# Kernel tuning notes

Hardware: AMD Instinct MI355X
Metric: run time of the kernel (lower is better)

The kernel has to match this reference:

```python
import jax, jax.numpy as jnp
import numpy as np

B = 8192        # number of drug-cell pairs (graphs)
NPG = 32        # nodes per graph
EPG = 64        # directed edges per graph
N = B * NPG     # total nodes
E = B * EPG     # total edges
CELL = 908      # cell_inp_dim
BN_EPS = 1e-5


def _bn(x):
    # BatchNorm1d in training mode with gamma=1, beta=0 (fresh init), biased var
    m = x.mean(0)
    v = x.var(0)
    return (x - m) * jax.lax.rsqrt(v + BN_EPS)


def _lin_params(k, fan_in, fan_out):
    kw, _ = jax.random.split(k)
    w = jax.random.normal(kw, (fan_in, fan_out), jnp.float32) / np.sqrt(fan_in)
    b = jnp.zeros((fan_out,), jnp.float32)
    return w, b


_DIMS = [("ce_1", CELL, 516), ("ce_2", 516, 256), ("ce_3", 256, 128),
         ("g1_1", 9, 128), ("g1_2", 128, 128),
         ("g2_1", 128, 128), ("g2_2", 128, 128),
         ("d_1", 128, 128), ("d_2", 128, 128),
         ("f_1", 256, 128), ("f_2", 128, 64), ("f_3", 64, 1)]


def setup_inputs() -> dict:
    key = jax.random.key(0)
    ks = jax.random.split(key, 4 + len(_DIMS))
    inp = {}
    inp["cell"] = jax.random.normal(ks[0], (B, CELL), jnp.float32)
    inp["drug_x"] = jax.random.normal(ks[1], (N, 9), jnp.float32)
    g = jnp.arange(E) // EPG  # graph id per edge
    src = g * NPG + jax.random.randint(ks[2], (E,), 0, NPG)
    dst = g * NPG + jax.random.randint(ks[3], (E,), 0, NPG)
    inp["drug_edge_index"] = jnp.stack([src, dst]).astype(jnp.int32)
    inp["drug_batch"] = (jnp.arange(N) // NPG).astype(jnp.int32)
    for i, (nm, a, b) in enumerate(_DIMS):
        w, bb = _lin_params(ks[4 + i], a, b)
        inp[nm + "_w"] = w
        inp[nm + "_b"] = bb
    return inp


def _forward(cell, drug_x, src, dst, batch,
             ce_1_w, ce_1_b, ce_2_w, ce_2_b, ce_3_w, ce_3_b,
             g1_1_w, g1_1_b, g1_2_w, g1_2_b,
             g2_1_w, g2_1_b, g2_2_w, g2_2_b,
             d_1_w, d_1_b, d_2_w, d_2_b,
             f_1_w, f_1_b, f_2_w, f_2_b, f_3_w, f_3_b):
    # cell_emb branch (dropout = identity in eval/reference)
    c = jax.nn.relu(_bn(cell @ ce_1_w + ce_1_b))
    c = jax.nn.relu(_bn(c @ ce_2_w + ce_2_b))
    c = jax.nn.relu(_bn(c @ ce_3_w + ce_3_b))

    # GINConv 1: h = MLP((1+eps)*x + sum_{j in N(i)} x_j), eps=0
    agg = jax.ops.segment_sum(drug_x[src], dst, num_segments=N)
    h = drug_x + agg
    h = jax.nn.relu(_bn(h @ g1_1_w + g1_1_b)) @ g1_2_w + g1_2_b  # inner MLP: Lin-BN-ReLU-Lin
    h = _bn(jax.nn.relu(h))  # outer ReLU then BN (per Sequential order)

    # GINConv 2
    agg = jax.ops.segment_sum(h[src], dst, num_segments=N)
    h = h + agg
    h = jax.nn.relu(_bn(h @ g2_1_w + g2_1_b)) @ g2_2_w + g2_2_b
    h = _bn(jax.nn.relu(h))

    # global max pool over nodes of each graph -> [B, 128]
    p = jax.ops.segment_max(h, batch, num_segments=B)

    d = jax.nn.relu(_bn(p @ d_1_w + d_1_b))
    d = jax.nn.relu(d @ d_2_w + d_2_b)

    z = jnp.concatenate([c, d], axis=-1)  # [B, 256]
    z = jax.nn.elu(_bn(z @ f_1_w + f_1_b))
    z = jax.nn.elu(_bn(z @ f_2_w + f_2_b))
    y = (z @ f_3_w + f_3_b).reshape(B)
    return y


def reference(cell, drug_x, drug_edge_index, drug_batch,
              ce_1_w, ce_1_b, ce_2_w, ce_2_b, ce_3_w, ce_3_b,
              g1_1_w, g1_1_b, g1_2_w, g1_2_b,
              g2_1_w, g2_1_b, g2_2_w, g2_2_b,
              d_1_w, d_1_b, d_2_w, d_2_b,
              f_1_w, f_1_b, f_2_w, f_2_b, f_3_w, f_3_b):
    src, dst = drug_edge_index[0], drug_edge_index[1]
    return _forward(cell, drug_x, src, dst, drug_batch,
                    ce_1_w, ce_1_b, ce_2_w, ce_2_b, ce_3_w, ce_3_b,
                    g1_1_w, g1_1_b, g1_2_w, g1_2_b,
                    g2_1_w, g2_1_b, g2_2_w, g2_2_b,
                    d_1_w, d_1_b, d_2_w, d_2_b,
                    f_1_w, f_1_b, f_2_w, f_2_b, f_3_w, f_3_b)
```

## Files before the change

kernel.cpp:

```cpp
#include <hip/hip_runtime.h>
#include <hip/hip_bf16.h>
#include <math.h>

#define BGRAPH 8192
#define NPG 32
#define EPG 64
#define NNODE (BGRAPH * NPG)
#define NEDGE (BGRAPH * EPG)
#define CELLD 908
#define BN_EPS 1e-5f
#define ABF_STR 1024
#define C1_STR 640

typedef __attribute__((ext_vector_type(8))) short bf16x8;
typedef __attribute__((ext_vector_type(4))) float f32x4;
typedef __attribute__((ext_vector_type(4))) unsigned short us4;
typedef __attribute__((ext_vector_type(8))) unsigned short us8;

__device__ __forceinline__ unsigned short f2bf(float f)
{
    unsigned int u = __float_as_uint(f);
    u = (u + 0x7FFFu + ((u >> 16) & 1u)) >> 16;
    return (unsigned short)u;
}

__device__ __forceinline__ bf16x8 quant8(const float v[8])
{
    union { bf16x8 b; unsigned short u[8]; } fr;
    #pragma unroll
    for (int j = 0; j < 8; ++j) fr.u[j] = f2bf(v[j]);
    return fr.b;
}

__device__ __forceinline__ void bf2f8(bf16x8 b, float v[8])
{
    union { bf16x8 bb; unsigned short u[8]; } x; x.bb = b;
    #pragma unroll
    for (int j = 0; j < 8; ++j) v[j] = __uint_as_float((unsigned)x.u[j] << 16);
}

__device__ __forceinline__ float apply_in(float v, int mode, float mn, float iv)
{
    if (mode == 1)      { v = (v - mn) * iv; v = fmaxf(v, 0.f); }
    else if (mode == 2) { v = (v - mn) * iv; v = (v > 0.f) ? v : expm1f(v); }
    else if (mode == 3) { v = fmaxf(v, 0.f); v = (v - mn) * iv; }
    return v;
}

struct TransArgs {
    const float* w[11];
    unsigned short* wt[11];
    int K[11], N[11], ntN[11];
    int off[12];
};

__global__ void transpose_w(TransArgs a)
{
    __shared__ float t[64][65];
    int b = blockIdx.x, tid = threadIdx.x;
    int s = 0;
    while (s < 10 && b >= a.off[s + 1]) ++s;
    int t0 = b - a.off[s];
    int K = a.K[s], N = a.N[s], ntn = a.ntN[s];
    int kt = t0 / ntn, nt = t0 - kt * ntn;
    int k0 = kt * 64, n0 = nt * 64;
    const float* w = a.w[s];
    unsigned short* wt = a.wt[s];
    int c = tid & 63, rg = tid >> 6;
    #pragma unroll
    for (int i = 0; i < 16; ++i) {
        int rr = rg * 16 + i;
        int k = k0 + rr, n = n0 + c;
        t[c][rr] = (k < K && n < N) ? w[(size_t)k * N + n] : 0.f;
    }
    __syncthreads();
    #pragma unroll
    for (int i = 0; i < 16; ++i) {
        int rr = rg * 16 + i;
        int n = n0 + rr, k = k0 + c;
        if (n < N && k < K) wt[(size_t)n * K + k] = f2bf(t[rr][c]);
    }
}

struct SetupArgs {
    float* zb; int zTotal; int zBlocks;
    const int* src; const int* dst; int* row_start; int* col_idx;
};

__global__ void setup_all(SetupArgs a)
{
    int b = blockIdx.x;
    int tid = threadIdx.x;
    if (b < a.zBlocks) {
        int i = b * 256 + tid;
        if (i < a.zTotal) a.zb[i] = 0.f;
        return;
    }
    b -= a.zBlocks;
    __shared__ int cnt[4][32], fill[4][32], rsl[4][33];
    int gl = tid >> 6, e = tid & 63;
    int g = b * 4 + gl;
    if (e < 32) { cnt[gl][e] = 0; fill[gl][e] = 0; }
    __syncthreads();
    int s = a.src[g * EPG + e] - g * NPG;
    int d = a.dst[g * EPG + e] - g * NPG;
    atomicAdd(&cnt[gl][d], 1);
    __syncthreads();
    if (e == 0) {
        int acc = 0;
        for (int i = 0; i < 32; ++i) { rsl[gl][i] = acc; acc += cnt[gl][i]; }
        rsl[gl][32] = acc;
    }
    __syncthreads();
    int pos = rsl[gl][d] + atomicAdd(&fill[gl][d], 1);
    a.col_idx[g * EPG + pos] = s;
    if (e < 33) a.row_start[g * 33 + e] = rsl[gl][e];
}

__global__ void quant_cell(const float* __restrict__ cell, unsigned short* __restrict__ abf)
{
    int i = blockIdx.x * 256 + threadIdx.x;
    int row = i / (ABF_STR / 4), c4 = i - row * (ABF_STR / 4);
    int k = c4 * 4;
    us4 w = (us4){0, 0, 0, 0};
    if (k < CELLD) {
        float4 f = *(const float4*)&cell[(size_t)row * CELLD + k];
        w = (us4){ f2bf(f.x), f2bf(f.y), f2bf(f.z), f2bf(f.w) };
    }
    *(us4*)&abf[(size_t)row * ABF_STR + k] = w;
}

__global__ void quant_c1(const float* __restrict__ c1, const float* __restrict__ stats,
                         float inv_sM, unsigned short* __restrict__ out)
{
    int i = blockIdx.x * 256 + threadIdx.x;
    int row = i / (C1_STR / 4), c4 = i - row * (C1_STR / 4);
    int k = c4 * 4;
    us4 w = (us4){0, 0, 0, 0};
    if (k < 516) {
        float4 f = *(const float4*)&c1[(size_t)row * 516 + k];
        float v[4] = {f.x, f.y, f.z, f.w};
        #pragma unroll
        for (int j = 0; j < 4; ++j) {
            float s = stats[k + j], ss = stats[516 + k + j];
            float mn = s * inv_sM;
            float iv = rsqrtf(ss * inv_sM - mn * mn + BN_EPS);
            v[j] = fmaxf((v[j] - mn) * iv, 0.f);
        }
        w = (us4){ f2bf(v[0]), f2bf(v[1]), f2bf(v[2]), f2bf(v[3]) };
    }
    *(us4*)&out[(size_t)row * C1_STR + k] = w;
}

__global__ void reduce_stats(const float* __restrict__ part, int nrows, int nt,
                             float* __restrict__ out)
{
    int c = threadIdx.x;
    int per = nrows >> 6;
    int r0 = blockIdx.x * per;
    bool isq = (c >= 128);
    int cc = isq ? c - 128 : c;
    if (cc >= nt) return;
    float s = 0.f;
    for (int r = 0; r < per; ++r) s += part[(size_t)(r0 + r) * 256 + c];
    unsafeAtomicAdd(&out[(isq ? nt : 0) + cc], s);
}

#define HBS 136

__launch_bounds__(256)
__global__ void gin_s1(const float* __restrict__ drug_x,
                       const int* __restrict__ row_start,
                       const int* __restrict__ col_idx,
                       const unsigned short* __restrict__ W11,
                       const float* __restrict__ b11,
                       unsigned short* uout,
                       float* __restrict__ part)
{
    __shared__ __align__(16) unsigned short h[4 * 32 * HBS];
    __shared__ __align__(16) unsigned char ubuf[4096];
    __shared__ int rs[4][36];
    __shared__ int ci[4][64];

    unsigned short* w11l = (unsigned short*)ubuf;
    float* red = (float*)ubuf;

    int tid  = threadIdx.x;
    int wave = tid >> 6;
    int lane = tid & 63;
    int quad = lane >> 4;
    int l16  = lane & 15;
    int g0   = blockIdx.x * 4;
    unsigned short* hw = h + wave * (32 * HBS);
    float* xw = (float*)hw;

    for (int i = tid; i < 128 * 16; i += 256) {
        int n = i >> 4, k = i & 15;
        w11l[i] = (k < 9) ? W11[n * 9 + k] : (unsigned short)0;
    }
    if (tid < 132) {
        int gl = tid / 33, idx = tid - gl * 33;
        rs[gl][idx] = row_start[(g0 + gl) * 33 + idx];
    }
    {
        int gl = tid >> 6, e = tid & 63;
        ci[gl][e] = col_idx[(g0 + gl) * EPG + e];
    }
    {
        const float* xg = drug_x + (size_t)(g0 + wave) * 32 * 9;
        for (int i = lane; i < 32 * 16; i += 64) {
            int rr = i >> 4, c = i & 15;
            xw[i] = (c < 9) ? xg[rr * 9 + c] : 0.f;
        }
    }
    __syncthreads();

    f32x4 acc[2][8];
    #pragma unroll
    for (int i = 0; i < 2; ++i)
        #pragma unroll
        for (int j = 0; j < 8; ++j)
            acc[i][j] = (f32x4){0.f, 0.f, 0.f, 0.f};

    {
        bf16x8 af[2];
        #pragma unroll
        for (int mt = 0; mt < 2; ++mt) {
            int rowl = mt * 16 + l16;
            float v[8] = {0, 0, 0, 0, 0, 0, 0, 0};
            if (quad < 2) {
                float4 lo = *(const float4*)&xw[rowl * 16 + quad * 8];
                float4 hi = *(const float4*)&xw[rowl * 16 + quad * 8 + 4];
                v[0] = lo.x; v[1] = lo.y; v[2] = lo.z; v[3] = lo.w;
                v[4] = hi.x; v[5] = hi.y; v[6] = hi.z; v[7] = hi.w;
                int e0 = rs[wave][rowl], e1 = rs[wave][rowl + 1];
                for (int e = e0; e < e1; ++e) {
                    int sr = ci[wave][e];
                    float4 l2 = *(const float4*)&xw[sr * 16 + quad * 8];
                    float4 h2 = *(const float4*)&xw[sr * 16 + quad * 8 + 4];
                    v[0] += l2.x; v[1] += l2.y; v[2] += l2.z; v[3] += l2.w;
                    v[4] += h2.x; v[5] += h2.y; v[6] += h2.z; v[7] += h2.w;
                }
            }
            af[mt] = quant8(v);
        }
        #pragma unroll
        for (int nt = 0; nt < 8; ++nt) {
            bf16x8 b;
            if (quad < 2) b = *(const bf16x8*)(const void*)&w11l[(nt * 16 + l16) * 16 + quad * 8];
            else { float z[8] = {0,0,0,0,0,0,0,0}; b = quant8(z); }
            acc[0][nt] = __builtin_amdgcn_mfma_f32_16x16x32_bf16(af[0], b, acc[0][nt], 0, 0, 0);
            acc[1][nt] = __builtin_amdgcn_mfma_f32_16x16x32_bf16(af[1], b, acc[1][nt], 0, 0, 0);
        }
    }

    float ls[8], lq[8];
    unsigned short* ub = uout + (size_t)(g0 + wave) * 32 * 128;
    #pragma unroll
    for (int nt = 0; nt < 8; ++nt) {
        int col = nt * 16 + l16;
        float bv = b11[col];
        float s0 = 0.f, q0 = 0.f;
        #pragma unroll
        for (int mt = 0; mt < 2; ++mt) {
            int rb = mt * 16 + quad * 4;
            #pragma unroll
            for (int r = 0; r < 4; ++r) {
                float u = acc[mt][nt][r] + bv;
                ub[(size_t)(rb + r) * 128 + col] = f2bf(u);
                s0 += u; q0 += u * u;
            }
        }
        ls[nt] = s0; lq[nt] = q0;
    }
    __syncthreads();
    #pragma unroll
    for (int nt = 0; nt < 8; ++nt) {
        float s = ls[nt], q = lq[nt];
        s += __shfl_xor(s, 16); q += __shfl_xor(q, 16);
        s += __shfl_xor(s, 32); q += __shfl_xor(q, 32);
        if (quad == 0) {
            int col = nt * 16 + l16;
            red[(wave * 2 + 0) * 128 + col] = s;
            red[(wave * 2 + 1) * 128 + col] = q;
        }
    }
    __syncthreads();
    if (tid < 128) {
        float s = red[0 * 128 + tid] + red[2 * 128 + tid] + red[4 * 128 + tid] + red[6 * 128 + tid];
        float q = red[1 * 128 + tid] + red[3 * 128 + tid] + red[5 * 128 + tid] + red[7 * 128 + tid];
        part[(size_t)blockIdx.x * 256 + tid] = s;
        part[(size_t)blockIdx.x * 256 + 128 + tid] = q;
    }
}

__launch_bounds__(256)
__global__ void gin_s3f(const unsigned short* __restrict__ uin,
                        const int* __restrict__ row_start,
                        const int* __restrict__ col_idx,
                        const unsigned short* __restrict__ Wt,
                        const float* __restrict__ bias,
                        const float* __restrict__ in_stats, float inv_sM,
                        unsigned short* __restrict__ uout,
                        float* __restrict__ part)
{
    __shared__ __align__(16) unsigned short wsl[128 * 136];
    __shared__ float pmv[256];
    __shared__ int rs[2][33];
    __shared__ int ci[2][64];
    float* zt = (float*)wsl;

    int tid  = threadIdx.x;
    int wave = tid >> 6;
    int lane = tid & 63;
    int quad = lane >> 4;
    int l16  = lane & 15;
    int g0   = blockIdx.x * 2;
    int row0 = blockIdx.x * 64;

    if (tid < 128) {
        float s = in_stats[tid], ss = in_stats[128 + tid];
        float mn = s * inv_sM;
        pmv[tid] = mn;
        pmv[128 + tid] = rsqrtf(ss * inv_sM - mn * mn + BN_EPS);
    }
    if (tid < 66) {
        int gl = tid / 33, idx = tid - gl * 33;
        rs[gl][idx] = row_start[(g0 + gl) * 33 + idx];
    }
    if (tid >= 128) {
        int t = tid - 128;
        ci[t >> 6][t & 63] = col_idx[(g0 + (t >> 6)) * EPG + (t & 63)];
    }
    for (int i = tid; i < 128 * 32; i += 256) {
        int n = i >> 5, k = (i & 31) * 4;
        *(us4*)&wsl[n * 136 + k] = *(const us4*)&Wt[(size_t)n * 128 + k];
    }
    __syncthreads();

    bf16x8 afrag[4];
    {
        const unsigned short* ap = uin + (size_t)(row0 + wave * 16 + l16) * 128;
        #pragma unroll
        for (int ks = 0; ks < 4; ++ks) {
            int kb = ks * 32 + quad * 8;
            float v[8];
            bf2f8(*(const bf16x8*)(const void*)&ap[kb], v);
            #pragma unroll
            for (int j = 0; j < 8; ++j)
                v[j] = (fmaxf(v[j], 0.f) - pmv[kb + j]) * pmv[128 + kb + j];
            afrag[ks] = quant8(v);
        }
    }

    f32x4 acc[8];
    #pragma unroll
    for (int j = 0; j < 8; ++j) acc[j] = (f32x4){0.f, 0.f, 0.f, 0.f};
    #pragma unroll
    for (int ks = 0; ks < 4; ++ks) {
        int kb = ks * 32 + quad * 8;
        #pragma unroll
        for (int nt = 0; nt < 8; ++nt) {
            bf16x8 b = *(const bf16x8*)(const void*)&wsl[(nt * 16 + l16) * 136 + kb];
            acc[nt] = __builtin_amdgcn_mfma_f32_16x16x32_bf16(afrag[ks], b, acc[nt], 0, 0, 0);
        }
    }
    __syncthreads();

    #pragma unroll
    for (int nt = 0; nt < 8; ++nt) {
        int col = nt * 16 + l16;
        #pragma unroll
        for (int r = 0; r < 4; ++r)
            zt[(wave * 16 + quad * 4 + r) * 132 + col] = acc[nt][r];
    }
    __syncthreads();

    float sv[4] = {0.f, 0.f, 0.f, 0.f}, qv[4] = {0.f, 0.f, 0.f, 0.f};
    {
        int c4  = (tid & 31) * 4;
        int rg  = tid >> 5;
        int hh  = rg >> 2;
        int rb0 = (rg & 3) * 8;
        float4 bv = *(const float4*)&bias[c4];
        unsigned short* ub = uout + (size_t)row0 * 128;
        for (int rr = 0; rr < 8; ++rr) {
            int r = rb0 + rr;
            int lr = hh * 32 + r;
            float4 val = *(const float4*)&zt[lr * 132 + c4];
            int e0 = rs[hh][r], e1 = rs[hh][r + 1];
            for (int e = e0; e < e1; ++e) {
                float4 zz = *(const float4*)&zt[(hh * 32 + ci[hh][e]) * 132 + c4];
                val.x += zz.x; val.y += zz.y; val.z += zz.z; val.w += zz.w;
            }
            float u0 = val.x + bv.x, u1 = val.y + bv.y;
            float u2 = val.z + bv.z, u3 = val.w + bv.w;
            *(us4*)&ub[(size_t)lr * 128 + c4] =
                (us4){ f2bf(u0), f2bf(u1), f2bf(u2), f2bf(u3) };
            sv[0] += u0; sv[1] += u1; sv[2] += u2; sv[3] += u3;
            qv[0] += u0 * u0; qv[1] += u1 * u1; qv[2] += u2 * u2; qv[3] += u3 * u3;
        }
    }
    __syncthreads();
    {
        int c4 = (tid & 31) * 4, rg = tid >> 5;
        #pragma unroll
        for (int j = 0; j < 4; ++j) {
            zt[rg * 128 + c4 + j] = sv[j];
            zt[1024 + rg * 128 + c4 + j] = qv[j];
        }
    }
    __syncthreads();
    if (tid < 128) {
        float s = 0.f, q = 0.f;
        #pragma unroll
        for (int rg = 0; rg < 8; ++rg) {
            s += zt[rg * 128 + tid];
            q += zt[1024 + rg * 128 + tid];
        }
        part[(size_t)blockIdx.x * 256 + tid] = s;
        part[(size_t)blockIdx.x * 256 + 128 + tid] = q;
    }
}

template<int DO_POOL>
__launch_bounds__(256)
__global__ void gin_lin(const unsigned short* __restrict__ uin,
                        const unsigned short* __restrict__ Wt,
                        const float* __restrict__ bias,
                        const float* __restrict__ in_stats, float inv_sM,
                        unsigned short* uout,
                        float* __restrict__ part,
                        float* __restrict__ pool_out)
{
    __shared__ __align__(16) unsigned short Ws_l[128 * 136];
    __shared__ float pmv[256];
    __shared__ float red[4][2][128];

    int tid  = threadIdx.x;
    int wave = tid >> 6;
    int lane = tid & 63;
    int quad = lane >> 4;
    int l16  = lane & 15;
    int row0 = blockIdx.x * 64;

    for (int i = tid; i < 128 * 32; i += 256) {
        int n = i >> 5, k = (i & 31) * 4;
        *(us4*)&Ws_l[n * 136 + k] = *(const us4*)&Wt[(size_t)n * 128 + k];
    }
    if (tid < 128) {
        float s = in_stats[tid], ss = in_stats[128 + tid];
        float mn = s * inv_sM;
        pmv[tid] = mn;
        pmv[128 + tid] = rsqrtf(ss * inv_sM - mn * mn + BN_EPS);
    }
    __syncthreads();

    bf16x8 afrag[4];
    {
        const unsigned short* ap = uin + (size_t)(row0 + wave * 16 + l16) * 128;
        #pragma unroll
        for (int ks = 0; ks < 4; ++ks) {
            int kb = ks * 32 + quad * 8;
            float v[8];
            bf2f8(*(const bf16x8*)(const void*)&ap[kb], v);
            #pragma unroll
            for (int j = 0; j < 8; ++j)
                v[j] = fmaxf((v[j] - pmv[kb + j]) * pmv[128 + kb + j], 0.f);
            afrag[ks] = quant8(v);
        }
    }

    f32x4 acc[8];
    #pragma unroll
    for (int j = 0; j < 8; ++j) acc[j] = (f32x4){0.f, 0.f, 0.f, 0.f};
    #pragma unroll
    for (int ks = 0; ks < 4; ++ks) {
        int kb = ks * 32 + quad * 8;
        #pragma unroll
        for (int nt = 0; nt < 8; ++nt) {
            bf16x8 b = *(const bf16x8*)(const void*)&Ws_l[(nt * 16 + l16) * 136 + kb];
            acc[nt] = __builtin_amdgcn_mfma_f32_16x16x32_bf16(afrag[ks], b, acc[nt], 0, 0, 0);
        }
    }

    float ls[8], lq[8], lm[8];
    #pragma unroll
    for (int nt = 0; nt < 8; ++nt) {
        int col = nt * 16 + l16;
        float bv = bias[col];
        int rb = row0 + wave * 16 + quad * 4;
        float s0 = 0.f, q0 = 0.f, mx = -INFINITY;
        #pragma unroll
        for (int r = 0; r < 4; ++r) {
            float u = acc[nt][r] + bv;
            float ru = fmaxf(u, 0.f);
            s0 += ru; q0 += ru * ru;
            if (DO_POOL) mx = fmaxf(mx, ru);
            else uout[(size_t)(rb + r) * 128 + col] = f2bf(u);
        }
        ls[nt] = s0; lq[nt] = q0; lm[nt] = mx;
    }

    #pragma unroll
    for (int nt = 0; nt < 8; ++nt) {
        float s = ls[nt], q = lq[nt];
        s += __shfl_xor(s, 16); q += __shfl_xor(q, 16);
        s += __shfl_xor(s, 32); q += __shfl_xor(q, 32);
        if (quad == 0) {
            red[wave][0][nt * 16 + l16] = s;
            red[wave][1][nt * 16 + l16] = q;
        }
    }
    __syncthreads();
    if (tid < 128) {
        float s = red[0][0][tid] + red[1][0][tid] + red[2][0][tid] + red[3][0][tid];
        float q = red[0][1][tid] + red[1][1][tid] + red[2][1][tid] + red[3][1][tid];
        part[(size_t)blockIdx.x * 256 + tid] = s;
        part[(size_t)blockIdx.x * 256 + 128 + tid] = q;
    }
    if (DO_POOL) {
        __syncthreads();
        #pragma unroll
        for (int nt = 0; nt < 8; ++nt) {
            float m = lm[nt];
            m = fmaxf(m, __shfl_xor(m, 16));
            m = fmaxf(m, __shfl_xor(m, 32));
            if (quad == 0) red[wave][0][nt * 16 + l16] = m;
        }
        __syncthreads();
        {
            int gi = tid >> 7, col = tid & 127;
            float m = fmaxf(red[gi * 2][0][col], red[gi * 2 + 1][0][col]);
            pool_out[(size_t)((row0 >> 5) + gi) * 128 + col] = m;
        }
    }
}

template<int KSTEPS, int NT>
__launch_bounds__(256)
__global__ void gemm_rB(const float* __restrict__ A, const float* __restrict__ A2,
                        int lda, int K, int stats_K, int ksplit,
                        const unsigned short* __restrict__ Wt,
                        const float* __restrict__ bias, float* __restrict__ C,
                        const float* __restrict__ in_stats, float inv_sM, int in_mode,
                        float* __restrict__ part, int stats_mode, int out_act)
{
    constexpr int NSUBW = NT / 64;
    __shared__ float pm[KSTEPS * 32], pv[KSTEPS * 32];

    int tid  = threadIdx.x;
    int wave = tid >> 6;
    int lane = tid & 63;
    int quad = lane >> 4;
    int l16  = lane & 15;
    int m0   = blockIdx.x * 16;

    if (in_mode) {
        for (int k = tid; k < KSTEPS * 32; k += 256) {
            float mn = 0.f, iv = 1.f;
            if (k < stats_K) {
                float s = in_stats[k], ss = in_stats[stats_K + k];
                mn = s * inv_sM;
                float vr = ss * inv_sM - mn * mn;
                iv = rsqrtf(vr + BN_EPS);
            }
            pm[k] = mn; pv[k] = iv;
        }
        __syncthreads();
    }

    bf16x8 afrag[KSTEPS];
    {
        int row = m0 + l16;
        const float* ap = A + (size_t)row * lda;
        #pragma unroll
        for (int ks = 0; ks < KSTEPS; ++ks) {
            int kb = ks * 32 + quad * 8;
            float v[8];
            #pragma unroll
            for (int hh = 0; hh < 2; ++hh) {
                int k = kb + hh * 4;
                const float* p = (k >= ksplit) ? &A2[(size_t)row * 128 + (k - 128)]
                                               : &ap[k];
                float4 f = *(const float4*)p;
                v[hh * 4 + 0] = f.x; v[hh * 4 + 1] = f.y;
                v[hh * 4 + 2] = f.z; v[hh * 4 + 3] = f.w;
            }
            if (in_mode) {
                #pragma unroll
                for (int j = 0; j < 8; ++j)
                    v[j] = apply_in(v[j], in_mode, pm[kb + j], pv[kb + j]);
            }
            afrag[ks] = quant8(v);
        }
    }

    f32x4 acc[NSUBW];
    #pragma unroll
    for (int j = 0; j < NSUBW; ++j) acc[j] = (f32x4){0.f, 0.f, 0.f, 0.f};

    #pragma unroll
    for (int ks = 0; ks < KSTEPS; ++ks) {
        #pragma unroll
        for (int nt = 0; nt < NSUBW; ++nt) {
            int wrow = (wave * NSUBW + nt) * 16 + l16;
            bf16x8 b = *(const bf16x8*)(const void*)&Wt[(size_t)wrow * K + ks * 32 + quad * 8];
            acc[nt] = __builtin_amdgcn_mfma_f32_16x16x32_bf16(afrag[ks], b, acc[nt], 0, 0, 0);
        }
    }

    float ls[NSUBW], lq[NSUBW];
    #pragma unroll
    for (int nt = 0; nt < NSUBW; ++nt) { ls[nt] = 0.f; lq[nt] = 0.f; }

    #pragma unroll
    for (int nt = 0; nt < NSUBW; ++nt) {
        int col = (wave * NSUBW + nt) * 16 + l16;
        float bv = bias[col];
        int rbase = m0 + quad * 4;
        #pragma unroll
        for (int r = 0; r < 4; ++r) {
            float u = acc[nt][r] + bv;
            if (C) {
                float wv = out_act ? fmaxf(u, 0.f) : u;
                C[(size_t)(rbase + r) * NT + col] = wv;
            }
            if (stats_mode) {
                float s = (stats_mode == 2) ? fmaxf(u, 0.f) : u;
                ls[nt] += s; lq[nt] += s * s;
            }
        }
    }

    if (stats_mode) {
        #pragma unroll
        for (int nt = 0; nt < NSUBW; ++nt) {
            float s = ls[nt], q = lq[nt];
            s += __shfl_xor(s, 16); q += __shfl_xor(q, 16);
            s += __shfl_xor(s, 32); q += __shfl_xor(q, 32);
            if (quad == 0) {
                int col = (wave * NSUBW + nt) * 16 + l16;
                part[(size_t)blockIdx.x * 256 + col] = s;
                part[(size_t)blockIdx.x * 256 + 128 + col] = q;
            }
        }
    }
}

template<int NT>
__launch_bounds__(256)
__global__ void gemm_cell(const unsigned short* __restrict__ Abf, int abf_str,
                          const unsigned short* __restrict__ Wt,
                          const float* __restrict__ bias, float* __restrict__ C,
                          int K, int N, float* __restrict__ out_stats)
{
    constexpr int NSUB = NT / 32;
    constexpr int WITEMS = NT * 32 / 256;
    __shared__ __align__(16) unsigned short As_l[32 * 136];
    __shared__ __align__(16) unsigned short Ws_l[NT * 136];
    __shared__ float red[2][2][NT];

    int tid = threadIdx.x;
    int wave = tid >> 6;
    int lane = tid & 63;
    int quad = lane >> 4;
    int l16 = lane & 15;
    int mhalf = wave & 1, nhalf = wave >> 1;
    int m0 = blockIdx.x * 32, n0 = blockIdx.y * NT;

    us8 aReg[2];
    us4 wReg[WITEMS];

    auto loadA = [&](int k0) {
        #pragma unroll
        for (int t = 0; t < 2; ++t) {
            int i = t * 256 + tid;
            int row = i >> 4, c8 = (i & 15) * 8;
            aReg[t] = *(const us8*)&Abf[(size_t)(m0 + row) * abf_str + k0 + c8];
        }
    };
    auto loadW = [&](int k0) {
        #pragma unroll
        for (int t = 0; t < WITEMS; ++t) {
            int i = t * 256 + tid;
            int nn = i >> 5, kt = i & 31;
            int k = k0 + kt * 4;
            int gn = n0 + nn;
            us4 w4 = (us4){0, 0, 0, 0};
            if (gn < N && k < K) w4 = *(const us4*)&Wt[(size_t)gn * K + k];
            wReg[t] = w4;
        }
    };
    auto storeAW = [&]() {
        #pragma unroll
        for (int t = 0; t < 2; ++t) {
            int i = t * 256 + tid;
            int row = i >> 4, c8 = (i & 15) * 8;
            *(us8*)&As_l[row * 136 + c8] = aReg[t];
        }
        #pragma unroll
        for (int t = 0; t < WITEMS; ++t) {
            int i = t * 256 + tid;
            int nn = i >> 5, kt = i & 31;
            *(us4*)&Ws_l[nn * 136 + kt * 4] = wReg[t];
        }
    };

    f32x4 acc[NSUB];
    #pragma unroll
    for (int j = 0; j < NSUB; ++j) acc[j] = (f32x4){0.f, 0.f, 0.f, 0.f};

    int nch = (K + 127) >> 7;
    loadA(0); loadW(0);
    for (int c = 0; c < nch; ++c) {
        storeAW();
        if (c + 1 < nch) { loadA((c + 1) * 128); loadW((c + 1) * 128); }
        __syncthreads();
        #pragma unroll
        for (int ks = 0; ks < 4; ++ks) {
            bf16x8 a = *(const bf16x8*)(const void*)
                &As_l[(mhalf * 16 + l16) * 136 + ks * 32 + quad * 8];
            #pragma unroll
            for (int nt = 0; nt < NSUB; ++nt) {
                bf16x8 b = *(const bf16x8*)(const void*)
                    &Ws_l[(nhalf * (NT / 2) + nt * 16 + l16) * 136 + ks * 32 + quad * 8];
                acc[nt] = __builtin_amdgcn_mfma_f32_16x16x32_bf16(a, b, acc[nt], 0, 0, 0);
            }
        }
        __syncthreads();
    }

    float ls[NSUB], lq[NSUB];
    #pragma unroll
    for (int nt = 0; nt < NSUB; ++nt) { ls[nt] = 0.f; lq[nt] = 0.f; }

    #pragma unroll
    for (int nt = 0; nt < NSUB; ++nt) {
        int col = n0 + nhalf * (NT / 2) + nt * 16 + l16;
        if (col < N) {
            float bv = bias[col];
            int rbase = m0 + mhalf * 16 + quad * 4;
            #pragma unroll
            for (int r = 0; r < 4; ++r) {
                float u = acc[nt][r] + bv;
                C[(size_t)(rbase + r) * N + col] = u;
                ls[nt] += u; lq[nt] += u * u;
            }
        }
    }

    #pragma unroll
    for (int nt = 0; nt < NSUB; ++nt) {
        float s = ls[nt], q = lq[nt];
        s += __shfl_xor(s, 16); q += __shfl_xor(q, 16);
        s += __shfl_xor(s, 32); q += __shfl_xor(q, 32);
        if (quad == 0) {
            int lc = nhalf * (NT / 2) + nt * 16 + l16;
            red[mhalf][0][lc] = s;
            red[mhalf][1][lc] = q;
        }
    }
    __syncthreads();
    if (tid < NT) {
        int col = n0 + tid;
        if (col < N) {
            float s = red[0][0][tid] + red[1][0][tid];
            float q = red[0][1][tid] + red[1][1][tid];
            unsafeAtomicAdd(&out_stats[col], s);
            unsafeAtomicAdd(&out_stats[N + col], q);
        }
    }
}

__global__ void final_dot(const float* __restrict__ u, const float* __restrict__ w,
                          const float* __restrict__ b, float* __restrict__ y,
                          const float* __restrict__ stats, float inv_sM)
{
    __shared__ float pmv[64], piv[64], sw[64];
    int tid = threadIdx.x;
    if (tid < 64) {
        float s = stats[tid], ss = stats[64 + tid];
        float mn = s * inv_sM;
        float vr = ss * inv_sM - mn * mn;
        pmv[tid] = mn;
        piv[tid] = rsqrtf(vr + BN_EPS);
        sw[tid] = w[tid];
    }
    __syncthreads();
    int i = blockIdx.x * blockDim.x + tid;
    if (i >= BGRAPH) return;
    float acc = 0.f;
    #pragma unroll
    for (int k = 0; k < 64; ++k) {
        float v = (u[(size_t)i * 64 + k] - pmv[k]) * piv[k];
        v = (v > 0.f) ? v : expm1f(v);
        acc += v * sw[k];
    }
    y[i] = acc + b[0];
}

extern "C" void kernel_launch(void* const* d_in, const int* in_sizes, int n_in,
                              void* d_out, int out_size, void* d_ws, size_t ws_size,
                              hipStream_t stream)
{
    const float* cell   = (const float*)d_in[0];
    const float* drug_x = (const float*)d_in[1];
    const int*   eidx   = (const int*)d_in[2];
    const float* ce1w = (const float*)d_in[4];  const float* ce1b = (const float*)d_in[5];
    const float* ce2w = (const float*)d_in[6];  const float* ce2b = (const float*)d_in[7];
    const float* ce3w = (const float*)d_in[8];  const float* ce3b = (const float*)d_in[9];
    const float* g11w = (const float*)d_in[10]; const float* g11b = (const float*)d_in[11];
    const float* g12w = (const float*)d_in[12]; const float* g12b = (const float*)d_in[13];
    const float* g21w = (const float*)d_in[14]; const float* g21b = (const float*)d_in[15];
    const float* g22w = (const float*)d_in[16]; const float* g22b = (const float*)d_in[17];
    const float* d1w  = (const float*)d_in[18]; const float* d1b  = (const float*)d_in[19];
    const float* d2w  = (const float*)d_in[20]; const float* d2b  = (const float*)d_in[21];
    const float* f1w  = (const float*)d_in[22]; const float* f1b  = (const float*)d_in[23];
    const float* f2w  = (const float*)d_in[24]; const float* f2b  = (const float*)d_in[25];
    const float* f3w  = (const float*)d_in[26]; const float* f3b  = (const float*)d_in[27];

    const int* src = eidx;
    const int* dst = eidx + NEDGE;
    float* out = (float*)d_out;

    const float INV_N = 1.f / (float)NNODE;
    const float INV_B = 1.f / (float)BGRAPH;
    const int KBIG = 1 << 30;

    float* ws = (float*)d_ws;
    unsigned short* ubg = (unsigned short*)ws;
    float* pbuf = ws + (size_t)NNODE * 64;
    float* sb   = pbuf + (size_t)BGRAPH * 128;
    unsigned short* wtb = (unsigned short*)(sb + 10 * 1032);
    auto ST = [&](int i) { return sb + (size_t)i * 1032; };
    float* st_u1    = ST(0);
    float* st_u2rel = ST(1);
    float* st_u3    = ST(2);
    float* st_u4rel = ST(3);
    float* st_c1    = ST(4);
    float* st_c2    = ST(5);
    float* st_c3    = ST(6);
    float* st_d1    = ST(7);
    float* st_f1    = ST(8);
    float* st_f2    = ST(9);

    float* c1    = ws;
    float* c2    = c1 + (size_t)BGRAPH * 516;
    float* c3u   = c2 + (size_t)BGRAPH * 256;
    float* dbuf  = c3u + (size_t)BGRAPH * 128;
    float* d2buf = dbuf + (size_t)BGRAPH * 128;
    float* f1o   = d2buf + (size_t)BGRAPH * 128;
    float* f2o   = f1o + (size_t)BGRAPH * 128;

    struct WDef { const float* w; int K; int N; };
    WDef wd[11] = {
        {ce1w, CELLD, 516}, {ce2w, 516, 256}, {ce3w, 256, 128},
        {g11w, 9, 128}, {g12w, 128, 128}, {g21w, 128, 128}, {g22w, 128, 128},
        {d1w, 128, 128}, {d2w, 128, 128}, {f1w, 256, 128}, {f2w, 128, 64}
    };
    TransArgs ta;
    int off = 0;
    unsigned short* wt[11];
    ta.off[0] = 0;
    for (int i = 0; i < 11; ++i) {
        wt[i] = wtb + off;
        ta.w[i] = wd[i].w; ta.wt[i] = wt[i];
        ta.K[i] = wd[i].K; ta.N[i] = wd[i].N;
        ta.ntN[i] = (wd[i].N + 63) / 64;
        ta.off[i + 1] = ta.off[i] + ((wd[i].K + 63) / 64) * ta.ntN[i];
        off += wd[i].K * wd[i].N;
    }

    SetupArgs sa;
    sa.zb = sb; sa.zTotal = 10 * 1032; sa.zBlocks = (10 * 1032 + 255) / 256;
    sa.src = src; sa.dst = dst;

    int csr_off = (off + 7) & ~7;
    int* row_start = (int*)(wtb + csr_off);
    int* col_idx   = row_start + (size_t)BGRAPH * 33;
    float* part = (float*)(col_idx + (size_t)NEDGE);
    unsigned short* Abf  = (unsigned short*)(part + (size_t)4096 * 256);
    unsigned short* C1bf = Abf + (size_t)BGRAPH * ABF_STR;
    sa.row_start = row_start; sa.col_idx = col_idx;

    transpose_w<<<ta.off[11], 256, 0, stream>>>(ta);
    setup_all<<<sa.zBlocks + BGRAPH / 4, 256, 0, stream>>>(sa);

    gin_s1<<<BGRAPH / 4, 256, 0, stream>>>(
        drug_x, row_start, col_idx, wt[3], g11b, ubg, part);
    reduce_stats<<<64, 256, 0, stream>>>(part, BGRAPH / 4, 128, st_u1);

    gin_lin<0><<<NNODE / 64, 256, 0, stream>>>(
        ubg, wt[4], g12b, st_u1, INV_N, ubg, part, nullptr);
    reduce_stats<<<64, 256, 0, stream>>>(part, NNODE / 64, 128, st_u2rel);

    gin_s3f<<<BGRAPH / 2, 256, 0, stream>>>(
        ubg, row_start, col_idx, wt[5], g21b, st_u2rel, INV_N, ubg, part);
    reduce_stats<<<64, 256, 0, stream>>>(part, BGRAPH / 2, 128, st_u3);

    gin_lin<1><<<NNODE / 64, 256, 0, stream>>>(
        ubg, wt[6], g22b, st_u3, INV_N, nullptr, part, pbuf);
    reduce_stats<<<64, 256, 0, stream>>>(part, NNODE / 64, 128, st_u4rel);

    quant_cell<<<(BGRAPH * (ABF_STR / 4)) / 256, 256, 0, stream>>>(cell, Abf);
    gemm_cell<128><<<dim3(BGRAPH / 32, 5), 256, 0, stream>>>(
        Abf, ABF_STR, wt[0], ce1b, c1, CELLD, 516, st_c1);
    quant_c1<<<(BGRAPH * (C1_STR / 4)) / 256, 256, 0, stream>>>(c1, st_c1, INV_B, C1bf);
    gemm_cell<64><<<dim3(BGRAPH / 32, 4), 256, 0, stream>>>(
        C1bf, C1_STR, wt[1], ce2b, c2, 516, 256, st_c2);
    gemm_rB<8, 128><<<BGRAPH / 16, 256, 0, stream>>>(
        c2, nullptr, 256, 256, 256, KBIG, wt[2], ce3b, c3u,
        st_c2, INV_B, 1, part, 1, 0);
    reduce_stats<<<64, 256, 0, stream>>>(part, BGRAPH / 16, 128, st_c3);

    gemm_rB<4, 128><<<BGRAPH / 16, 256, 0, stream>>>(
        pbuf, nullptr, 128, 128, 128, KBIG, wt[7], d1b, dbuf,
        st_u4rel, INV_N, 3, part, 1, 0);
    reduce_stats<<<64, 256, 0, stream>>>(part, BGRAPH / 16, 128, st_d1);
    gemm_rB<4, 128><<<BGRAPH / 16, 256, 0, stream>>>(
        dbuf, nullptr, 128, 128, 128, KBIG, wt[8], d2b, d2buf,
        st_d1, INV_B, 1, part, 0, 1);

    gemm_rB<8, 128><<<BGRAPH / 16, 256, 0, stream>>>(
        c3u, d2buf, 128, 256, 128, 128, wt[9], f1b, f1o,
        st_c3, INV_B, 1, part, 1, 0);
    reduce_stats<<<64, 256, 0, stream>>>(part, BGRAPH / 16, 128, st_f1);
    gemm_rB<4, 64><<<BGRAPH / 16, 256, 0, stream>>>(
        f1o, nullptr, 128, 128, 128, KBIG, wt[10], f2b, f2o,
        st_f1, INV_B, 2, part, 1, 0);
    reduce_stats<<<64, 256, 0, stream>>>(part, BGRAPH / 16, 64, st_f2);
    final_dot<<<BGRAPH / 256, 256, 0, stream>>>(f2o, f3w, f3b, out, st_f2, INV_B);
}
```

Before: 525.9 us.

## Drop LDS weight staging in GIN kernels and shrink s3f blocks to one graph

The GIN layer kernels no longer copy the 128x128 bf16 weight matrix into shared memory and instead read MFMA B fragments directly from global memory, relying on L1/L2 caching. gin_s3f is also restructured to process one graph per block, 32 rows, with four waves split over M and N halves. This doubles its grid and shrinks its LDS footprint, so the partial-stats buffer and the Abf offset grow to match. The aim is to remove the per-block weight staging and the syncs around it and to raise occupancy. The cost is more global/L1 load traffic for weights, possibly uncoalesced fragment loads, and twice as many partial rows to reduce.

```diff
diff --git a/kernel.cpp b/kernel.cpp
--- a/kernel.cpp
+++ b/kernel.cpp
@@ -304,19 +304,20 @@
                         unsigned short* __restrict__ uout,
                         float* __restrict__ part)
 {
-    __shared__ __align__(16) unsigned short wsl[128 * 136];
+    __shared__ __align__(16) float zt[32 * 132];
     __shared__ float pmv[256];
-    __shared__ int rs[2][33];
-    __shared__ int ci[2][64];
-    float* zt = (float*)wsl;
+    __shared__ int rs[33];
+    __shared__ int ci[64];
 
     int tid  = threadIdx.x;
     int wave = tid >> 6;
     int lane = tid & 63;
     int quad = lane >> 4;
     int l16  = lane & 15;
-    int g0   = blockIdx.x * 2;
-    int row0 = blockIdx.x * 64;
+    int mh   = wave & 1;
+    int nh   = wave >> 1;
+    int g    = blockIdx.x;
+    int row0 = g * 32;
 
     if (tid < 128) {
         float s = in_stats[tid], ss = in_stats[128 + tid];
@@ -324,23 +325,13 @@
         pmv[tid] = mn;
         pmv[128 + tid] = rsqrtf(ss * inv_sM - mn * mn + BN_EPS);
     }
-    if (tid < 66) {
-        int gl = tid / 33, idx = tid - gl * 33;
-        rs[gl][idx] = row_start[(g0 + gl) * 33 + idx];
-    }
-    if (tid >= 128) {
-        int t = tid - 128;
-        ci[t >> 6][t & 63] = col_idx[(g0 + (t >> 6)) * EPG + (t & 63)];
-    }
-    for (int i = tid; i < 128 * 32; i += 256) {
-        int n = i >> 5, k = (i & 31) * 4;
-        *(us4*)&wsl[n * 136 + k] = *(const us4*)&Wt[(size_t)n * 128 + k];
-    }
+    if (tid >= 128 && tid < 161) rs[tid - 128] = row_start[g * 33 + (tid - 128)];
+    if (tid >= 192) ci[tid - 192] = col_idx[g * EPG + (tid - 192)];
     __syncthreads();
 
     bf16x8 afrag[4];
     {
-        const unsigned short* ap = uin + (size_t)(row0 + wave * 16 + l16) * 128;
+        const unsigned short* ap = uin + (size_t)(row0 + mh * 16 + l16) * 128;
         #pragma unroll
         for (int ks = 0; ks < 4; ++ks) {
             int kb = ks * 32 + quad * 8;
@@ -353,26 +344,26 @@
         }
     }
 
-    f32x4 acc[8];
-    #pragma unroll
-    for (int j = 0; j < 8; ++j) acc[j] = (f32x4){0.f, 0.f, 0.f, 0.f};
+    f32x4 acc[4];
+    #pragma unroll
+    for (int j = 0; j < 4; ++j) acc[j] = (f32x4){0.f, 0.f, 0.f, 0.f};
     #pragma unroll
     for (int ks = 0; ks < 4; ++ks) {
         int kb = ks * 32 + quad * 8;
         #pragma unroll
-        for (int nt = 0; nt < 8; ++nt) {
-            bf16x8 b = *(const bf16x8*)(const void*)&wsl[(nt * 16 + l16) * 136 + kb];
+        for (int nt = 0; nt < 4; ++nt) {
+            int wrow = nh * 64 + nt * 16 + l16;
+            bf16x8 b = *(const bf16x8*)(const void*)&Wt[(size_t)wrow * 128 + kb];
             acc[nt] = __builtin_amdgcn_mfma_f32_16x16x32_bf16(afrag[ks], b, acc[nt], 0, 0, 0);
         }
     }
-    __syncthreads();
-
-    #pragma unroll
-    for (int nt = 0; nt < 8; ++nt) {
-        int col = nt * 16 + l16;
+
+    #pragma unroll
+    for (int nt = 0; nt < 4; ++nt) {
+        int col = nh * 64 + nt * 16 + l16;
         #pragma unroll
         for (int r = 0; r < 4; ++r)
-            zt[(wave * 16 + quad * 4 + r) * 132 + col] = acc[nt][r];
+            zt[(mh * 16 + quad * 4 + r) * 132 + col] = acc[nt][r];
     }
     __syncthreads();
 
@@ -380,22 +371,19 @@
     {
         int c4  = (tid & 31) * 4;
         int rg  = tid >> 5;
-        int hh  = rg >> 2;
-        int rb0 = (rg & 3) * 8;
         float4 bv = *(const float4*)&bias[c4];
         unsigned short* ub = uout + (size_t)row0 * 128;
-        for (int rr = 0; rr < 8; ++rr) {
-            int r = rb0 + rr;
-            int lr = hh * 32 + r;
-            float4 val = *(const float4*)&zt[lr * 132 + c4];
-            int e0 = rs[hh][r], e1 = rs[hh][r + 1];
+        for (int rr = 0; rr < 4; ++rr) {
+            int r = rg * 4 + rr;
+            float4 val = *(const float4*)&zt[r * 132 + c4];
+            int e0 = rs[r], e1 = rs[r + 1];
             for (int e = e0; e < e1; ++e) {
-                float4 zz = *(const float4*)&zt[(hh * 32 + ci[hh][e]) * 132 + c4];
+                float4 zz = *(const float4*)&zt[ci[e] * 132 + c4];
                 val.x += zz.x; val.y += zz.y; val.z += zz.z; val.w += zz.w;
             }
             float u0 = val.x + bv.x, u1 = val.y + bv.y;
             float u2 = val.z + bv.z, u3 = val.w + bv.w;
-            *(us4*)&ub[(size_t)lr * 128 + c4] =
+            *(us4*)&ub[(size_t)r * 128 + c4] =
                 (us4){ f2bf(u0), f2bf(u1), f2bf(u2), f2bf(u3) };
             sv[0] += u0; sv[1] += u1; sv[2] += u2; sv[3] += u3;
             qv[0] += u0 * u0; qv[1] += u1 * u1; qv[2] += u2 * u2; qv[3] += u3 * u3;
@@ -433,7 +421,6 @@
                         float* __restrict__ part,
                         float* __restrict__ pool_out)
 {
-    __shared__ __align__(16) unsigned short Ws_l[128 * 136];
     __shared__ float pmv[256];
     __shared__ float red[4][2][128];
 
@@ -444,10 +431,6 @@
     int l16  = lane & 15;
     int row0 = blockIdx.x * 64;
 
-    for (int i = tid; i < 128 * 32; i += 256) {
-        int n = i >> 5, k = (i & 31) * 4;
-        *(us4*)&Ws_l[n * 136 + k] = *(const us4*)&Wt[(size_t)n * 128 + k];
-    }
     if (tid < 128) {
         float s = in_stats[tid], ss = in_stats[128 + tid];
         float mn = s * inv_sM;
@@ -479,7 +462,7 @@
         int kb = ks * 32 + quad * 8;
         #pragma unroll
         for (int nt = 0; nt < 8; ++nt) {
-            bf16x8 b = *(const bf16x8*)(const void*)&Ws_l[(nt * 16 + l16) * 136 + kb];
+            bf16x8 b = *(const bf16x8*)(const void*)&Wt[(size_t)(nt * 16 + l16) * 128 + kb];
             acc[nt] = __builtin_amdgcn_mfma_f32_16x16x32_bf16(afrag[ks], b, acc[nt], 0, 0, 0);
         }
     }
@@ -880,7 +863,7 @@
     int* row_start = (int*)(wtb + csr_off);
     int* col_idx   = row_start + (size_t)BGRAPH * 33;
     float* part = (float*)(col_idx + (size_t)NEDGE);
-    unsigned short* Abf  = (unsigned short*)(part + (size_t)4096 * 256);
+    unsigned short* Abf  = (unsigned short*)(part + (size_t)8192 * 256);
     unsigned short* C1bf = Abf + (size_t)BGRAPH * ABF_STR;
     sa.row_start = row_start; sa.col_idx = col_idx;
 
@@ -895,9 +878,9 @@
         ubg, wt[4], g12b, st_u1, INV_N, ubg, part, nullptr);
     reduce_stats<<<64, 256, 0, stream>>>(part, NNODE / 64, 128, st_u2rel);
 
-    gin_s3f<<<BGRAPH / 2, 256, 0, stream>>>(
+    gin_s3f<<<BGRAPH, 256, 0, stream>>>(
         ubg, row_start, col_idx, wt[5], g21b, st_u2rel, INV_N, ubg, part);
-    reduce_stats<<<64, 256, 0, stream>>>(part, BGRAPH / 2, 128, st_u3);
+    reduce_stats<<<64, 256, 0, stream>>>(part, BGRAPH, 128, st_u3);
 
     gin_lin<1><<<NNODE / 64, 256, 0, stream>>>(
         ubg, wt[6], g22b, st_u3, INV_N, nullptr, part, pbuf);
```

New measurement: 644.2 us. 1.22x slower.
